# Performance work log

Measured on AMD Instinct MI355X. Metric: run time of the kernel, lower is better.

Reference implementation:

```python
import jax, jax.numpy as jnp
import numpy as np

N_NODES = 100000
N_TARGETS = 8192
HIDDEN = 128
HEADS = 4


def setup_inputs() -> dict:
    key = jax.random.key(0)
    ks = iter(jax.random.split(key, 40))
    d = {}
    d['feat0'] = jax.random.normal(next(ks), (50000, 512), jnp.float32)
    d['feat1'] = jax.random.normal(next(ks), (50000, 512), jnp.float32)
    d['node_idx0'] = jnp.arange(50000, dtype=jnp.int32)
    d['node_idx1'] = jnp.arange(50000, dtype=jnp.int32) + 50000
    for nt in ('m', 'd'):
        for p in ('0', '1'):
            d[f'eidx_{nt}{p}'] = jax.random.randint(next(ks), (100000, 3), 0, N_NODES, jnp.int32)
            d[f'etgt_{nt}{p}'] = jax.random.randint(next(ks), (100000,), 0, N_TARGETS, jnp.int32)
    s = lambda *sh: 0.05 * jax.random.normal(next(ks), sh, jnp.float32)
    d['W0'] = s(HIDDEN, 512); d['b0'] = jnp.zeros((HIDDEN,), jnp.float32)
    d['W1'] = s(HIDDEN, 512); d['b1'] = jnp.zeros((HIDDEN,), jnp.float32)
    for nt in ('m', 'd'):
        for p in ('0', '1'):
            d[f'Wr_{nt}{p}'] = s(HEADS * HIDDEN, HIDDEN)
            d[f'a_{nt}{p}'] = s(HEADS, HIDDEN)
        d[f'Ws_{nt}'] = s(128, HEADS * HIDDEN)
        d[f'bs_{nt}'] = jnp.zeros((128,), jnp.float32)
        d[f'vs_{nt}'] = s(128)
        d[f'Wo_{nt}'] = s(64, HEADS * HIDDEN)
        d[f'bo_{nt}'] = jnp.zeros((64,), jnp.float32)
    return d


def _metapath_agg(feats, eidx, etgt, Wr, attn):
    # feats: [N,H]; eidx: [E,L]; etgt: [E] in [0,T)
    E = eidx.shape[0]
    h = feats[eidx].mean(axis=1)                       # [E,H]  metapath-instance encoding ('linear' rnn_type)
    eft = (h @ Wr.T).reshape(E, HEADS, HIDDEN)         # [E,heads,H]
    e = jax.nn.leaky_relu(jnp.einsum('ehd,hd->eh', eft, attn), 0.2)
    m = jax.ops.segment_max(e, etgt, num_segments=N_TARGETS)
    ex = jnp.exp(e - m[etgt])
    den = jax.ops.segment_sum(ex, etgt, num_segments=N_TARGETS)
    alpha = ex / (den[etgt] + 1e-9)                    # segment softmax over instances per target
    out = jax.ops.segment_sum(eft * alpha[:, :, None], etgt, num_segments=N_TARGETS)
    return jax.nn.elu(out).reshape(N_TARGETS, HEADS * HIDDEN)


def _semantic(h_list, Ws, bs, vs):
    betas = jnp.stack([(jnp.tanh(h @ Ws.T + bs) @ vs).mean() for h in h_list])
    beta = jax.nn.softmax(betas)
    return jnp.einsum('p,pth->th', beta, jnp.stack(h_list))


def reference(feat0, feat1, node_idx0, node_idx1,
              eidx_m0, etgt_m0, eidx_m1, etgt_m1,
              eidx_d0, etgt_d0, eidx_d1, etgt_d1,
              W0, b0, W1, b1,
              Wr_m0, a_m0, Wr_m1, a_m1, Wr_d0, a_d0, Wr_d1, a_d1,
              Ws_m, bs_m, vs_m, Ws_d, bs_d, vs_d,
              Wo_m, bo_m, Wo_d, bo_d):
    # per-node-type linear transform scattered by type_mask
    tf = jnp.zeros((N_NODES, HIDDEN), feat0.dtype)
    tf = tf.at[node_idx0].set(feat0 @ W0.T + b0)
    tf = tf.at[node_idx1].set(feat1 @ W1.T + b1)
    # (feat_drop is identity in eval / dropout_rate handled deterministically)
    hm0 = _metapath_agg(tf, eidx_m0, etgt_m0, Wr_m0, a_m0)
    hm1 = _metapath_agg(tf, eidx_m1, etgt_m1, Wr_m1, a_m1)
    hd0 = _metapath_agg(tf, eidx_d0, etgt_d0, Wr_d0, a_d0)
    hd1 = _metapath_agg(tf, eidx_d1, etgt_d1, Wr_d1, a_d1)
    h_miRNA = _semantic([hm0, hm1], Ws_m, bs_m, vs_m)
    h_disease = _semantic([hd0, hd1], Ws_d, bs_d, vs_d)
    logits_miRNA = h_miRNA @ Wo_m.T + bo_m
    logits_disease = h_disease @ Wo_d.T + bo_d
    return (logits_miRNA, logits_disease, h_miRNA, h_disease)
```

## Files before the change

### kernel.cpp

```cpp
#include <hip/hip_runtime.h>
#include <hip/hip_bf16.h>
#include <math.h>


#define HIDDEN 128
#define HEADS 4
#define NTGT 8192
#define NEDGE 100000
#define NNODES 100000

typedef __attribute__((ext_vector_type(8))) short bf16x8;
typedef __attribute__((ext_vector_type(4))) float f32x4;

__device__ inline short b16(float f)
{
    union { __hip_bfloat16 h; short s; } u;
    u.h = __float2bfloat16(f);
    return u.s;
}

__device__ inline float bf2f(unsigned short u)
{
    union { unsigned int i; float f; } v;
    v.i = (unsigned int)u << 16;
    return v.f;
}

struct GArgs {
    const void* A[4];
    const unsigned short* B[4];
    const float* bias[4];
    void* C[4];
    const int* rowmap[4];
    const float* vs[4];
    float* sem[4];
};

__global__ __launch_bounds__(256, 4)
void tgemm(GArgs g, int M)
{
    __shared__ unsigned short lds[32 * 512];
    const int z = blockIdx.z;
    const float* Af = (const float*)g.A[z];
    const unsigned short* Bp = g.B[z];
    const float* bias = g.bias[z];
    const int* rowmap = g.rowmap[z];
    unsigned short* Ch = (unsigned short*)g.C[z];

    const int tid = threadIdx.x;
    const int w = tid >> 6, l = tid & 63;
    const int lr = l & 15, s4 = l >> 4;
    const int m0 = blockIdx.x * 32;

    auto stage4 = [&](int rbase) {
        float4 v[4][2];
        #pragma unroll
        for (int q = 0; q < 4; ++q) {
            int rg = min(m0 + rbase + q, M - 1);
            const float* rowp = Af + (size_t)rg * 512;
            v[q][0] = *(const float4*)(rowp + l * 4);
            v[q][1] = *(const float4*)(rowp + 256 + l * 4);
        }
        #pragma unroll
        for (int q = 0; q < 4; ++q) {
            int rl = rbase + q;
            int rx = rl & 7;
            #pragma unroll
            for (int hh = 0; hh < 2; ++hh) {
                uint2 pk;
                pk.x = (unsigned int)(unsigned short)b16(v[q][hh].x) |
                       ((unsigned int)(unsigned short)b16(v[q][hh].y) << 16);
                pk.y = (unsigned int)(unsigned short)b16(v[q][hh].z) |
                       ((unsigned int)(unsigned short)b16(v[q][hh].w) << 16);
                int G = hh * 32 + (l >> 1);
                int slot = (G & ~7) | ((G & 7) ^ rx);
                *(uint2*)((char*)lds + (size_t)rl * 1024 + slot * 16 + (l & 1) * 8) = pk;
            }
        }
    };
    stage4(w * 8);
    stage4(w * 8 + 4);

    const int i = w & 1;
    const int jb = (w >> 1) * 4;

    f32x4 acc[4];
    #pragma unroll
    for (int jj = 0; jj < 4; ++jj) acc[jj] = (f32x4){0.f, 0.f, 0.f, 0.f};

    bf16x8 bbA[4], bbB[4];
    auto LDB = [&](int c, bf16x8 (&bb)[4]) {
        #pragma unroll
        for (int jj = 0; jj < 4; ++jj)
            bb[jj] = *(const bf16x8*)(Bp + ((size_t)(c * 8 + jb + jj) * 64 + l) * 8);
    };

    LDB(0, bbA);
    __syncthreads();

    const int r = i * 16 + lr;
    const int rx = r & 7;

    #pragma unroll
    for (int c = 0; c < 16; ++c) {
        int G = 4 * c + s4;
        int slot = (G & ~7) | ((G & 7) ^ rx);
        bf16x8 a = *(const bf16x8*)((const char*)lds + (size_t)r * 1024 + slot * 16);
        if (c & 1) {
            if (c + 1 < 16) LDB(c + 1, bbA);
            #pragma unroll
            for (int jj = 0; jj < 4; ++jj)
                acc[jj] = __builtin_amdgcn_mfma_f32_16x16x32_bf16(a, bbB[jj], acc[jj], 0, 0, 0);
        } else {
            if (c + 1 < 16) LDB(c + 1, bbB);
            #pragma unroll
            for (int jj = 0; jj < 4; ++jj)
                acc[jj] = __builtin_amdgcn_mfma_f32_16x16x32_bf16(a, bbA[jj], acc[jj], 0, 0, 0);
        }
    }

    #pragma unroll
    for (int rr = 0; rr < 4; ++rr) {
        int gm = m0 + i * 16 + s4 * 4 + rr;
        if (gm >= M) continue;
        size_t crow = (size_t)rowmap[gm];
        #pragma unroll
        for (int jj = 0; jj < 4; ++jj) {
            int n = (jb + jj) * 16 + lr;
            Ch[crow * 128 + n] = (unsigned short)b16(acc[jj][rr] + bias[n]);
        }
    }
}

template<int EPI, int NF, int MI, bool AB16, bool C16, int NFS>
__global__ __launch_bounds__(256)
void mgemm(GArgs g, int lda, int ldc,
           int aOffY, int bOffY, int cOffY, int nOffY, int M, int K)
{
    __shared__ float red[4];
    const int z = blockIdx.z;
    const unsigned short* Bp = g.B[z] + (size_t)blockIdx.y * bOffY;
    const float* bias = g.bias[z];
    const int* rowmap = g.rowmap[z];
    const int nbase = blockIdx.y * nOffY;
    float* Cf = nullptr;
    unsigned short* Ch = nullptr;
    if (g.C[z]) {
        if (C16) Ch = (unsigned short*)g.C[z] + (size_t)blockIdx.y * cOffY;
        else     Cf = (float*)g.C[z] + (size_t)blockIdx.y * cOffY;
    }
    const float* Af = nullptr;
    const unsigned short* Ah = nullptr;
    if (AB16) Ah = (const unsigned short*)g.A[z] + (size_t)blockIdx.y * aOffY;
    else      Af = (const float*)g.A[z] + (size_t)blockIdx.y * aOffY;

    const int tid = threadIdx.x;
    const int w = tid >> 6, l = tid & 63;
    const int lr = l & 15, lk = (l >> 4) * 8;
    const int m0 = blockIdx.x * (MI * 64) + w * (MI * 16);

    f32x4 acc[MI][NF];
    #pragma unroll
    for (int i = 0; i < MI; ++i)
        #pragma unroll
        for (int j = 0; j < NF; ++j)
            acc[i][j] = (f32x4){0.f, 0.f, 0.f, 0.f};

    float4 af0[MI][2], af1[MI][2];
    bf16x8 ah0[MI], ah1[MI];
    bf16x8 bb0[NF], bb1[NF];

    auto LD = [&](int k0, float4 (&af)[MI][2], bf16x8 (&ah)[MI], bf16x8 (&bb)[NF]) {
        #pragma unroll
        for (int i = 0; i < MI; ++i) {
            int row = min(m0 + i * 16 + lr, M - 1);
            if (AB16) {
                ah[i] = *(const bf16x8*)(Ah + (size_t)row * lda + k0 + lk);
            } else {
                const float* p = Af + (size_t)row * lda + k0 + lk;
                af[i][0] = *(const float4*)p;
                af[i][1] = *(const float4*)(p + 4);
            }
        }
        #pragma unroll
        for (int j = 0; j < NF; ++j)
            bb[j] = *(const bf16x8*)(Bp + ((size_t)((k0 >> 5) * NFS + j) * 64 + l) * 8);
    };

    auto CMP = [&](float4 (&af)[MI][2], bf16x8 (&ah)[MI], bf16x8 (&bb)[NF]) {
        bf16x8 a[MI];
        #pragma unroll
        for (int i = 0; i < MI; ++i) {
            if (AB16) {
                a[i] = ah[i];
            } else {
                bf16x8 r;
                r[0] = b16(af[i][0].x); r[1] = b16(af[i][0].y);
                r[2] = b16(af[i][0].z); r[3] = b16(af[i][0].w);
                r[4] = b16(af[i][1].x); r[5] = b16(af[i][1].y);
                r[6] = b16(af[i][1].z); r[7] = b16(af[i][1].w);
                a[i] = r;
            }
        }
        #pragma unroll
        for (int j = 0; j < NF; ++j)
            #pragma unroll
            for (int i = 0; i < MI; ++i)
                acc[i][j] = __builtin_amdgcn_mfma_f32_16x16x32_bf16(a[i], bb[j], acc[i][j], 0, 0, 0);
    };

    LD(0, af0, ah0, bb0);
    for (int k0 = 0; k0 < K; k0 += 64) {
        LD(k0 + 32, af1, ah1, bb1);
        CMP(af0, ah0, bb0);
        if (k0 + 64 < K) LD(k0 + 64, af0, ah0, bb0);
        CMP(af1, ah1, bb1);
    }

    if (EPI == 2) {
        const float* vs = g.vs[z];
        float local = 0.f;
        #pragma unroll
        for (int i = 0; i < MI; ++i) {
            int rbase = m0 + i * 16 + (l >> 4) * 4;
            #pragma unroll
            for (int r = 0; r < 4; ++r) {
                if (rbase + r >= M) continue;
                #pragma unroll
                for (int j = 0; j < NF; ++j) {
                    int n = nbase + j * 16 + lr;
                    local += tanhf(acc[i][j][r] + bias[n]) * vs[n];
                }
            }
        }
        #pragma unroll
        for (int o = 32; o; o >>= 1) local += __shfl_xor(local, o, 64);
        if (l == 0) red[w] = local;
        __syncthreads();
        if (tid == 0) atomicAdd(g.sem[z], red[0] + red[1] + red[2] + red[3]);
        return;
    }

    #pragma unroll
    for (int i = 0; i < MI; ++i) {
        int rbase = m0 + i * 16 + (l >> 4) * 4;
        #pragma unroll
        for (int r = 0; r < 4; ++r) {
            int gm = rbase + r;
            if (gm >= M) continue;
            size_t crow = rowmap ? (size_t)rowmap[gm] : (size_t)gm;
            #pragma unroll
            for (int j = 0; j < NF; ++j) {
                int n = nbase + j * 16 + lr;
                float v = acc[i][j][r];
                if (EPI == 0 && bias) v += bias[n];
                if (EPI == 1) v = v > 0.f ? v : expm1f(v);
                if (C16) Ch[crow * (size_t)ldc + n] = (unsigned short)b16(v);
                else     Cf[crow * (size_t)ldc + n] = v;
            }
        }
    }
}

struct PackArgs {
    const float* src[22];
    unsigned short* dst[22];
    int n16[22], k32[22], ld[22];
};

__global__ __launch_bounds__(256)
void pack_kernel(PackArgs pa)
{
    int c = blockIdx.y;
    int idx = blockIdx.x * 256 + threadIdx.x;
    int tot = pa.n16[c] * pa.k32[c] * 64;
    if (idx >= tot) return;
    int l = idx & 63;
    int rest = idx >> 6;
    int j = rest % pa.n16[c];
    int k0 = rest / pa.n16[c];
    int row = j * 16 + (l & 15);
    int col = k0 * 32 + (l >> 4) * 8;
    const float* s = pa.src[c] + (size_t)row * pa.ld[c] + col;
    float4 u = *(const float4*)s;
    float4 v = *(const float4*)(s + 4);
    bf16x8 r;
    r[0] = b16(u.x); r[1] = b16(u.y); r[2] = b16(u.z); r[3] = b16(u.w);
    r[4] = b16(v.x); r[5] = b16(v.y); r[6] = b16(v.z); r[7] = b16(v.w);
    *(bf16x8*)(pa.dst[c] + (size_t)idx * 8) = r;
}

struct WattArgs { const float* Wr[4]; const float* a[4]; };

__global__ __launch_bounds__(256)
void watt_kernel(WattArgs wa, float* __restrict__ watt4)
{
    int idx = blockIdx.x * 256 + threadIdx.x;
    int mp = idx >> 9, rest = idx & 511, h = rest >> 7, k = rest & 127;
    const float* Wr = wa.Wr[mp];
    const float* a = wa.a[mp];
    float s = 0.f;
    #pragma unroll 4
    for (int d = 0; d < HIDDEN; ++d)
        s += a[h * HIDDEN + d] * Wr[(size_t)(h * HIDDEN + d) * HIDDEN + k];
    watt4[idx] = s;
}

__global__ __launch_bounds__(256)
void watt_pack(const float* __restrict__ watt4, unsigned short* __restrict__ dst)
{
    int idx = blockIdx.x * 256 + threadIdx.x;
    int f = idx >> 9;
    int r = idx & 511;
    int l = r >> 3;
    int c = r & 7;
    int row = l & 15;
    int col = f * 32 + ((l >> 4) << 3) + c;
    dst[idx] = (unsigned short)b16(watt4[row * 128 + col]);
}

struct EArgs { const int* eidx[4]; const int* etgt[4]; };

__global__ __launch_bounds__(256)
void hist_kernel(EArgs ea, int* __restrict__ cnt4, int E)
{
    int e = blockIdx.x * 256 + threadIdx.x;
    int mp = blockIdx.y;
    if (e < E) atomicAdd(&cnt4[mp * NTGT + ea.etgt[mp][e]], 1);
}

__global__ __launch_bounds__(256)
void scan_kernel(int* __restrict__ cnt4, int* __restrict__ rowptr4)
{
    int mp = blockIdx.x;
    int* cnt = cnt4 + mp * NTGT;
    int* rowptr = rowptr4 + mp * (NTGT + 1);
    __shared__ int part[256];
    int t = threadIdx.x;
    int vals[32];
    int s = 0;
    int base = t * 32;
    #pragma unroll
    for (int i = 0; i < 32; ++i) { vals[i] = cnt[base + i]; s += vals[i]; }
    part[t] = s;
    __syncthreads();
    for (int o = 1; o < 256; o <<= 1) {
        int v = (t >= o) ? part[t - o] : 0;
        __syncthreads();
        part[t] += v;
        __syncthreads();
    }
    int off = (t == 0) ? 0 : part[t - 1];
    #pragma unroll
    for (int i = 0; i < 32; ++i) { rowptr[base + i] = off; off += vals[i]; cnt[base + i] = 0; }
    if (t == 255) rowptr[NTGT] = off;
}

__global__ __launch_bounds__(256)
void scatter_esc(EArgs ea, const int* __restrict__ rowptr4,
                 int* __restrict__ cur4, uint4* __restrict__ rec4,
                 const float* __restrict__ snode, int E)
{
    int e = blockIdx.x * 256 + threadIdx.x;
    int mp = blockIdx.y;
    if (e >= E) return;
    int t = ea.etgt[mp][e];
    int pos = atomicAdd(&cur4[mp * NTGT + t], 1);
    int slot = rowptr4[mp * (NTGT + 1) + t] + pos;

    const int* eidx = ea.eidx[mp];
    int i0 = eidx[e * 3 + 0], i1 = eidx[e * 3 + 1], i2 = eidx[e * 3 + 2];
    float4 s0 = *(const float4*)(snode + (size_t)i0 * 16 + mp * 4);
    float4 s1 = *(const float4*)(snode + (size_t)i1 * 16 + mp * 4);
    float4 s2 = *(const float4*)(snode + (size_t)i2 * 16 + mp * 4);
    const float inv3 = 1.f / 3.f;
    float es[4];
    es[0] = (s0.x + s1.x + s2.x) * inv3;
    es[1] = (s0.y + s1.y + s2.y) * inv3;
    es[2] = (s0.z + s1.z + s2.z) * inv3;
    es[3] = (s0.w + s1.w + s2.w) * inv3;
    #pragma unroll
    for (int h = 0; h < 4; ++h) {
        float v = (es[h] >= 0.f) ? es[h] : 0.2f * es[h];
        es[h] = __expf(v);
    }
    uint4* rp = rec4 + ((size_t)mp * NEDGE + slot) * 2;
    rp[0] = make_uint4((unsigned)i0, (unsigned)i1, (unsigned)i2, 0u);
    *(float4*)&rp[1] = make_float4(es[0], es[1], es[2], es[3]);
}

__global__ __launch_bounds__(256)
void seg_kernel(const int* __restrict__ rowptr4, const uint4* __restrict__ rec4,
                const unsigned short* __restrict__ tfb,
                unsigned short* __restrict__ gnb)
{
    int mp = blockIdx.y;
    int w = threadIdx.x >> 6, l = threadIdx.x & 63;
    int t = blockIdx.x * 4 + w;
    const int* rp = rowptr4 + mp * (NTGT + 1);
    const uint4* rec = rec4 + (size_t)mp * NEDGE * 2;
    const unsigned short* tfl = tfb + 2 * l;

    int beg = rp[t], end = rp[t + 1];
    int n = end - beg;
    float den[4] = {0, 0, 0, 0}, aa[4] = {0, 0, 0, 0}, ab[4] = {0, 0, 0, 0};
    const float inv3 = 1.f / 3.f;

    if (n > 0) {
        int last = n - 1;
        auto LDI = [&](int j, uint4& ia, float4& wv) {
            int jj = min(j, last);
            ia = rec[(size_t)(beg + jj) * 2];
            wv = *(const float4*)&rec[(size_t)(beg + jj) * 2 + 1];
        };
        uint4 I0, I1, I2, I3, I4;
        float4 W0v, W1v, W2v, W3v, W4v;
        LDI(0, I0, W0v); LDI(1, I1, W1v); LDI(2, I2, W2v); LDI(3, I3, W3v);
        unsigned int x0 = *(const unsigned int*)(tfl + (size_t)I0.x * 128);
        unsigned int x1 = *(const unsigned int*)(tfl + (size_t)I0.y * 128);
        unsigned int x2 = *(const unsigned int*)(tfl + (size_t)I0.z * 128);
        unsigned int y0 = *(const unsigned int*)(tfl + (size_t)I1.x * 128);
        unsigned int y1 = *(const unsigned int*)(tfl + (size_t)I1.y * 128);
        unsigned int y2 = *(const unsigned int*)(tfl + (size_t)I1.z * 128);
        unsigned int z0 = *(const unsigned int*)(tfl + (size_t)I2.x * 128);
        unsigned int z1 = *(const unsigned int*)(tfl + (size_t)I2.y * 128);
        unsigned int z2 = *(const unsigned int*)(tfl + (size_t)I2.z * 128);
        for (int i = 0; i < n; ++i) {
            unsigned int w0 = *(const unsigned int*)(tfl + (size_t)I3.x * 128);
            unsigned int w1 = *(const unsigned int*)(tfl + (size_t)I3.y * 128);
            unsigned int w2 = *(const unsigned int*)(tfl + (size_t)I3.z * 128);
            LDI(i + 4, I4, W4v);
            float fa = (bf2f((unsigned short)x0) + bf2f((unsigned short)x1) +
                        bf2f((unsigned short)x2)) * inv3;
            float fb = (bf2f((unsigned short)(x0 >> 16)) + bf2f((unsigned short)(x1 >> 16)) +
                        bf2f((unsigned short)(x2 >> 16))) * inv3;
            float es[4] = {W0v.x, W0v.y, W0v.z, W0v.w};
            #pragma unroll
            for (int h = 0; h < 4; ++h) {
                den[h] += es[h]; aa[h] += es[h] * fa; ab[h] += es[h] * fb;
            }
            x0 = y0; x1 = y1; x2 = y2;
            y0 = z0; y1 = z1; y2 = z2;
            z0 = w0; z1 = w1; z2 = w2;
            I3 = I4;
            W0v = W1v; W1v = W2v; W2v = W3v; W3v = W4v;
        }
    }

    unsigned short* gr = gnb + ((size_t)mp * NTGT + t) * 512;
    #pragma unroll
    for (int h = 0; h < 4; ++h) {
        float d = 1.f / (den[h] + 1e-9f);
        unsigned int lo = (unsigned int)(unsigned short)b16(aa[h] * d);
        unsigned int hi = (unsigned int)(unsigned short)b16(ab[h] * d);
        *(unsigned int*)(gr + h * 128 + 2 * l) = lo | (hi << 16);
    }
}

__global__ void beta_kernel(const float* __restrict__ s, float* __restrict__ beta)
{
    int nt = threadIdx.x;
    if (nt < 2 && blockIdx.x == 0) {
        float b0 = s[nt * 2] * (1.f / 8192.f), b1 = s[nt * 2 + 1] * (1.f / 8192.f);
        float mm = fmaxf(b0, b1);
        float e0 = __expf(b0 - mm), e1 = __expf(b1 - mm);
        float d = e0 + e1;
        beta[nt * 2] = e0 / d;
        beta[nt * 2 + 1] = e1 / d;
    }
}

__global__ __launch_bounds__(256)
void combine_kernel(const unsigned short* __restrict__ obb,
                    const float* __restrict__ betab,
                    float* __restrict__ hout, unsigned short* __restrict__ hb)
{
    int nt = blockIdx.y;
    size_t i4 = ((size_t)blockIdx.x * 256 + threadIdx.x) * 4;
    const unsigned short* o0 = obb + (size_t)(2 * nt) * NTGT * 512 + i4;
    const unsigned short* o1 = obb + (size_t)(2 * nt + 1) * NTGT * 512 + i4;
    float b0 = betab[nt * 2], b1 = betab[nt * 2 + 1];
    uint2 xa = *(const uint2*)o0;
    uint2 xb = *(const uint2*)o1;
    float4 r;
    r.x = b0 * bf2f((unsigned short)xa.x)         + b1 * bf2f((unsigned short)xb.x);
    r.y = b0 * bf2f((unsigned short)(xa.x >> 16)) + b1 * bf2f((unsigned short)(xb.x >> 16));
    r.z = b0 * bf2f((unsigned short)xa.y)         + b1 * bf2f((unsigned short)xb.y);
    r.w = b0 * bf2f((unsigned short)(xa.y >> 16)) + b1 * bf2f((unsigned short)(xb.y >> 16));
    *(float4*)(hout + (size_t)nt * NTGT * 512 + i4) = r;
    unsigned int lo = (unsigned int)(unsigned short)b16(r.x) |
                      ((unsigned int)(unsigned short)b16(r.y) << 16);
    unsigned int hi = (unsigned int)(unsigned short)b16(r.z) |
                      ((unsigned int)(unsigned short)b16(r.w) << 16);
    *(uint2*)(hb + (size_t)nt * NTGT * 512 + i4) = make_uint2(lo, hi);
}

extern "C" void kernel_launch(void* const* d_in, const int* in_sizes, int n_in,
                              void* d_out, int out_size, void* d_ws, size_t ws_size,
                              hipStream_t stream)
{
    const float* feat0 = (const float*)d_in[0];
    const float* feat1 = (const float*)d_in[1];
    const int* nidx0 = (const int*)d_in[2];
    const int* nidx1 = (const int*)d_in[3];
    const int* eidx[4] = {(const int*)d_in[4], (const int*)d_in[6],
                          (const int*)d_in[8], (const int*)d_in[10]};
    const int* etgt[4] = {(const int*)d_in[5], (const int*)d_in[7],
                          (const int*)d_in[9], (const int*)d_in[11]};
    const float* W0 = (const float*)d_in[12]; const float* b0 = (const float*)d_in[13];
    const float* W1 = (const float*)d_in[14]; const float* b1 = (const float*)d_in[15];
    const float* Wr[4] = {(const float*)d_in[16], (const float*)d_in[18],
                          (const float*)d_in[25], (const float*)d_in[27]};
    const float* av[4] = {(const float*)d_in[17], (const float*)d_in[19],
                          (const float*)d_in[26], (const float*)d_in[28]};
    const float* Ws[2] = {(const float*)d_in[20], (const float*)d_in[29]};
    const float* bs[2] = {(const float*)d_in[21], (const float*)d_in[30]};
    const float* vsem[2] = {(const float*)d_in[22], (const float*)d_in[31]};
    const float* Wo[2] = {(const float*)d_in[23], (const float*)d_in[32]};
    const float* bo[2] = {(const float*)d_in[24], (const float*)d_in[33]};
    float* out = (float*)d_out;

    char* p = (char*)d_ws;
    auto carve = [&](size_t bytes) { char* r = p; p += (bytes + 255) & ~(size_t)255; return r; };
    unsigned short* tfb = (unsigned short*)carve((size_t)NNODES * 128 * 2);
    unsigned short* gnb = (unsigned short*)carve((size_t)4 * NTGT * 512 * 2);
    unsigned short* obb = (unsigned short*)carve((size_t)4 * NTGT * 512 * 2);
    unsigned short* hb  = (unsigned short*)carve((size_t)2 * NTGT * 512 * 2);
    float* snode        = (float*)carve((size_t)NNODES * 16 * 4);
    uint4* rec4         = (uint4*)carve((size_t)4 * NEDGE * 32);
    unsigned short* w0b = (unsigned short*)carve(65536 * 2);
    unsigned short* w1b = (unsigned short*)carve(65536 * 2);
    unsigned short* wrb = (unsigned short*)carve(4 * 65536 * 2);
    unsigned short* wsb = (unsigned short*)carve(2 * 65536 * 2);
    unsigned short* wob = (unsigned short*)carve(2 * 32768 * 2);
    unsigned short* wattp = (unsigned short*)carve(2048 * 2);
    float* watt4        = (float*)carve(4 * 512 * 4);
    float* ssem         = (float*)carve(4 * 4);
    float* betab        = (float*)carve(4 * 4);
    int* cnt4           = (int*)carve((size_t)4 * NTGT * 4);
    int* rowptr4        = (int*)carve((size_t)4 * (NTGT + 1) * 4);

    hipMemsetAsync(ssem, 0, 16, stream);
    hipMemsetAsync(cnt4, 0, (size_t)4 * NTGT * 4, stream);

    dim3 blk(256, 1, 1);

    PackArgs pa;
    pa.src[0] = W0; pa.dst[0] = w0b; pa.n16[0] = 8; pa.k32[0] = 16; pa.ld[0] = 512;
    pa.src[1] = W1; pa.dst[1] = w1b; pa.n16[1] = 8; pa.k32[1] = 16; pa.ld[1] = 512;
    for (int mp = 0; mp < 4; ++mp)
        for (int h = 0; h < 4; ++h) {
            int c = 2 + mp * 4 + h;
            pa.src[c] = Wr[mp] + (size_t)h * 128 * 128;
            pa.dst[c] = wrb + (size_t)(mp * 4 + h) * 16384;
            pa.n16[c] = 8; pa.k32[c] = 4; pa.ld[c] = 128;
        }
    pa.src[18] = Ws[0]; pa.dst[18] = wsb;         pa.n16[18] = 8; pa.k32[18] = 16; pa.ld[18] = 512;
    pa.src[19] = Ws[1]; pa.dst[19] = wsb + 65536; pa.n16[19] = 8; pa.k32[19] = 16; pa.ld[19] = 512;
    pa.src[20] = Wo[0]; pa.dst[20] = wob;         pa.n16[20] = 4; pa.k32[20] = 16; pa.ld[20] = 512;
    pa.src[21] = Wo[1]; pa.dst[21] = wob + 32768; pa.n16[21] = 4; pa.k32[21] = 16; pa.ld[21] = 512;
    pack_kernel<<<dim3(32, 22), blk, 0, stream>>>(pa);

    WattArgs wa;
    for (int mp = 0; mp < 4; ++mp) { wa.Wr[mp] = Wr[mp]; wa.a[mp] = av[mp]; }
    watt_kernel<<<dim3(8), blk, 0, stream>>>(wa, watt4);
    watt_pack<<<dim3(8), blk, 0, stream>>>(watt4, wattp);

    {
        GArgs g = {};
        g.A[0] = feat0; g.A[1] = feat1;
        g.B[0] = w0b;   g.B[1] = w1b;
        g.bias[0] = b0; g.bias[1] = b1;
        g.C[0] = tfb;   g.C[1] = tfb;
        g.rowmap[0] = nidx0; g.rowmap[1] = nidx1;
        tgemm<<<dim3(1563, 1, 2), blk, 0, stream>>>(g, 50000);
    }

    {
        GArgs g = {};
        g.A[0] = tfb;
        g.B[0] = wattp;
        g.C[0] = snode;
        mgemm<0, 1, 2, true, false, 1><<<dim3(782, 1, 1), blk, 0, stream>>>(
            g, 128, 16, 0, 0, 0, 0, NNODES, 128);
    }

    EArgs ea;
    for (int mp = 0; mp < 4; ++mp) { ea.eidx[mp] = eidx[mp]; ea.etgt[mp] = etgt[mp]; }

    hist_kernel<<<dim3(391, 4), blk, 0, stream>>>(ea, cnt4, NEDGE);
    scan_kernel<<<dim3(4), blk, 0, stream>>>(cnt4, rowptr4);
    scatter_esc<<<dim3(391, 4), blk, 0, stream>>>(ea, rowptr4, cnt4, rec4,
                                                  snode, NEDGE);
    seg_kernel<<<dim3(NTGT / 4, 4), blk, 0, stream>>>(rowptr4, rec4, tfb, gnb);

    const size_t LOG_OFF[2] = {0, (size_t)NTGT * 64};
    float* hout = out + (size_t)NTGT * 128;

    {
        GArgs g = {};
        for (int mp = 0; mp < 4; ++mp) {
            g.A[mp] = gnb + (size_t)mp * NTGT * 512;
            g.B[mp] = wrb + (size_t)mp * 65536;
            g.C[mp] = obb + (size_t)mp * NTGT * 512;
        }
        mgemm<1, 8, 2, true, true, 8><<<dim3(64, 4, 4), blk, 0, stream>>>(
            g, 512, 512, 128, 16384, 128, 0, NTGT, 128);
    }

    {
        GArgs g = {};
        for (int mp = 0; mp < 4; ++mp) {
            int nt = mp >> 1;
            g.A[mp] = obb + (size_t)mp * NTGT * 512;
            g.B[mp] = wsb + (size_t)nt * 65536;
            g.bias[mp] = bs[nt];
            g.vs[mp] = vsem[nt];
            g.sem[mp] = ssem + mp;
        }
        mgemm<2, 4, 1, true, false, 8><<<dim3(128, 2, 4), blk, 0, stream>>>(
            g, 512, 0, 0, 2048, 0, 64, NTGT, 512);
    }

    beta_kernel<<<dim3(1), dim3(64), 0, stream>>>(ssem, betab);
    combine_kernel<<<dim3(NTGT * 512 / 4 / 256, 2), blk, 0, stream>>>(obb, betab, hout, hb);

    {
        GArgs g = {};
        for (int nt = 0; nt < 2; ++nt) {
            g.A[nt] = hb + (size_t)nt * NTGT * 512;
            g.B[nt] = wob + (size_t)nt * 32768;
            g.bias[nt] = bo[nt];
            g.C[nt] = out + LOG_OFF[nt];
        }
        mgemm<0, 2, 1, true, false, 4><<<dim3(128, 2, 2), blk, 0, stream>>>(
            g, 512, 64, 0, 1024, 0, 32, NTGT, 512);
    }
}
```

Before: 292.7 us.

## Make feature-transform GEMM persistent with register-prefetched 16-row tiles

The tgemm kernel becomes a persistent grid of 1280 blocks that loop over 16-row tiles covering both feature matrices. Each block prefetches the next tile's fp32 rows into registers while running MFMA on the current tile in LDS, so global loads overlap with compute. Tiles shrink from 32 rows to 16, and each wave now computes two output column groups instead of four, with a higher occupancy hint. The trade-off is more B-matrix reloads per row and an extra barrier per tile. The bounds checks are dropped because the tile count divides the row count exactly.

```diff
diff --git a/kernel.cpp b/kernel.cpp
--- a/kernel.cpp
+++ b/kernel.cpp
@@ -8,6 +8,10 @@
 #define NTGT 8192
 #define NEDGE 100000
 #define NNODES 100000
+#define TROWS 16
+#define TPF 3125
+#define NTILES (2 * TPF)
+#define TGRID 1280
 
 typedef __attribute__((ext_vector_type(8))) short bf16x8;
 typedef __attribute__((ext_vector_type(4))) float f32x4;
@@ -36,99 +40,104 @@
     float* sem[4];
 };
 
-__global__ __launch_bounds__(256, 4)
-void tgemm(GArgs g, int M)
-{
-    __shared__ unsigned short lds[32 * 512];
-    const int z = blockIdx.z;
-    const float* Af = (const float*)g.A[z];
-    const unsigned short* Bp = g.B[z];
-    const float* bias = g.bias[z];
-    const int* rowmap = g.rowmap[z];
-    unsigned short* Ch = (unsigned short*)g.C[z];
-
+__global__ __launch_bounds__(256, 5)
+void tgemm(GArgs g)
+{
+    __shared__ unsigned short lds[TROWS * 512];
     const int tid = threadIdx.x;
     const int w = tid >> 6, l = tid & 63;
     const int lr = l & 15, s4 = l >> 4;
-    const int m0 = blockIdx.x * 32;
-
-    auto stage4 = [&](int rbase) {
-        float4 v[4][2];
-        #pragma unroll
-        for (int q = 0; q < 4; ++q) {
-            int rg = min(m0 + rbase + q, M - 1);
-            const float* rowp = Af + (size_t)rg * 512;
-            v[q][0] = *(const float4*)(rowp + l * 4);
-            v[q][1] = *(const float4*)(rowp + 256 + l * 4);
-        }
-        #pragma unroll
-        for (int q = 0; q < 4; ++q) {
-            int rl = rbase + q;
+    const int jb = w * 2;
+
+    float4 v[8];
+
+    auto LOADR = [&](int t) {
+        int z = (t >= TPF) ? 1 : 0;
+        const float* Af = (const float*)g.A[z];
+        int rowbase = (t - z * TPF) * TROWS;
+        #pragma unroll
+        for (int q = 0; q < 8; ++q) {
+            int rl = w * 4 + (q >> 1);
+            v[q] = *(const float4*)(Af + (size_t)(rowbase + rl) * 512 +
+                                    (q & 1) * 256 + l * 4);
+        }
+    };
+
+    auto WRLDS = [&]() {
+        #pragma unroll
+        for (int q = 0; q < 8; ++q) {
+            int rl = w * 4 + (q >> 1);
             int rx = rl & 7;
-            #pragma unroll
-            for (int hh = 0; hh < 2; ++hh) {
-                uint2 pk;
-                pk.x = (unsigned int)(unsigned short)b16(v[q][hh].x) |
-                       ((unsigned int)(unsigned short)b16(v[q][hh].y) << 16);
-                pk.y = (unsigned int)(unsigned short)b16(v[q][hh].z) |
-                       ((unsigned int)(unsigned short)b16(v[q][hh].w) << 16);
-                int G = hh * 32 + (l >> 1);
-                int slot = (G & ~7) | ((G & 7) ^ rx);
-                *(uint2*)((char*)lds + (size_t)rl * 1024 + slot * 16 + (l & 1) * 8) = pk;
+            uint2 pk;
+            pk.x = (unsigned)(unsigned short)b16(v[q].x) |
+                   ((unsigned)(unsigned short)b16(v[q].y) << 16);
+            pk.y = (unsigned)(unsigned short)b16(v[q].z) |
+                   ((unsigned)(unsigned short)b16(v[q].w) << 16);
+            int G = (q & 1) * 32 + (l >> 1);
+            int slot = (G & ~7) | ((G & 7) ^ rx);
+            *(uint2*)((char*)lds + (size_t)rl * 1024 + slot * 16 + (l & 1) * 8) = pk;
+        }
+    };
+
+    auto COMPUTE = [&](int t) {
+        int z = (t >= TPF) ? 1 : 0;
+        const unsigned short* Bp = g.B[z];
+        const float* bias = g.bias[z];
+        const int* rowmap = g.rowmap[z];
+        unsigned short* Ch = (unsigned short*)g.C[z];
+        int rowbase = (t - z * TPF) * TROWS;
+
+        f32x4 acc0 = (f32x4){0.f, 0.f, 0.f, 0.f};
+        f32x4 acc1 = (f32x4){0.f, 0.f, 0.f, 0.f};
+        bf16x8 bA0, bA1, bB0, bB1;
+        bA0 = *(const bf16x8*)(Bp + ((size_t)(jb + 0) * 64 + l) * 8);
+        bA1 = *(const bf16x8*)(Bp + ((size_t)(jb + 1) * 64 + l) * 8);
+        const int r = lr, rx = r & 7;
+        #pragma unroll
+        for (int c = 0; c < 16; ++c) {
+            int G = 4 * c + s4;
+            int slot = (G & ~7) | ((G & 7) ^ rx);
+            bf16x8 a = *(const bf16x8*)((const char*)lds + (size_t)r * 1024 + slot * 16);
+            if (c & 1) {
+                if (c < 15) {
+                    bA0 = *(const bf16x8*)(Bp + ((size_t)((c + 1) * 8 + jb + 0) * 64 + l) * 8);
+                    bA1 = *(const bf16x8*)(Bp + ((size_t)((c + 1) * 8 + jb + 1) * 64 + l) * 8);
+                }
+                acc0 = __builtin_amdgcn_mfma_f32_16x16x32_bf16(a, bB0, acc0, 0, 0, 0);
+                acc1 = __builtin_amdgcn_mfma_f32_16x16x32_bf16(a, bB1, acc1, 0, 0, 0);
+            } else {
+                if (c < 15) {
+                    bB0 = *(const bf16x8*)(Bp + ((size_t)((c + 1) * 8 + jb + 0) * 64 + l) * 8);
+                    bB1 = *(const bf16x8*)(Bp + ((size_t)((c + 1) * 8 + jb + 1) * 64 + l) * 8);
+                }
+                acc0 = __builtin_amdgcn_mfma_f32_16x16x32_bf16(a, bA0, acc0, 0, 0, 0);
+                acc1 = __builtin_amdgcn_mfma_f32_16x16x32_bf16(a, bA1, acc1, 0, 0, 0);
             }
         }
+        #pragma unroll
+        for (int rr = 0; rr < 4; ++rr) {
+            int gm = rowbase + s4 * 4 + rr;
+            size_t crow = (size_t)rowmap[gm];
+            Ch[crow * 128 + (jb + 0) * 16 + lr] =
+                (unsigned short)b16(acc0[rr] + bias[(jb + 0) * 16 + lr]);
+            Ch[crow * 128 + (jb + 1) * 16 + lr] =
+                (unsigned short)b16(acc1[rr] + bias[(jb + 1) * 16 + lr]);
+        }
     };
-    stage4(w * 8);
-    stage4(w * 8 + 4);
-
-    const int i = w & 1;
-    const int jb = (w >> 1) * 4;
-
-    f32x4 acc[4];
-    #pragma unroll
-    for (int jj = 0; jj < 4; ++jj) acc[jj] = (f32x4){0.f, 0.f, 0.f, 0.f};
-
-    bf16x8 bbA[4], bbB[4];
-    auto LDB = [&](int c, bf16x8 (&bb)[4]) {
-        #pragma unroll
-        for (int jj = 0; jj < 4; ++jj)
-            bb[jj] = *(const bf16x8*)(Bp + ((size_t)(c * 8 + jb + jj) * 64 + l) * 8);
-    };
-
-    LDB(0, bbA);
-    __syncthreads();
-
-    const int r = i * 16 + lr;
-    const int rx = r & 7;
-
-    #pragma unroll
-    for (int c = 0; c < 16; ++c) {
-        int G = 4 * c + s4;
-        int slot = (G & ~7) | ((G & 7) ^ rx);
-        bf16x8 a = *(const bf16x8*)((const char*)lds + (size_t)r * 1024 + slot * 16);
-        if (c & 1) {
-            if (c + 1 < 16) LDB(c + 1, bbA);
-            #pragma unroll
-            for (int jj = 0; jj < 4; ++jj)
-                acc[jj] = __builtin_amdgcn_mfma_f32_16x16x32_bf16(a, bbB[jj], acc[jj], 0, 0, 0);
-        } else {
-            if (c + 1 < 16) LDB(c + 1, bbB);
-            #pragma unroll
-            for (int jj = 0; jj < 4; ++jj)
-                acc[jj] = __builtin_amdgcn_mfma_f32_16x16x32_bf16(a, bbA[jj], acc[jj], 0, 0, 0);
-        }
-    }
-
-    #pragma unroll
-    for (int rr = 0; rr < 4; ++rr) {
-        int gm = m0 + i * 16 + s4 * 4 + rr;
-        if (gm >= M) continue;
-        size_t crow = (size_t)rowmap[gm];
-        #pragma unroll
-        for (int jj = 0; jj < 4; ++jj) {
-            int n = (jb + jj) * 16 + lr;
-            Ch[crow * 128 + n] = (unsigned short)b16(acc[jj][rr] + bias[n]);
-        }
+
+    int tile = blockIdx.x;
+    if (tile >= NTILES) return;
+    LOADR(tile);
+    while (true) {
+        WRLDS();
+        __syncthreads();
+        int next = tile + TGRID;
+        bool more = (next < NTILES);
+        if (more) LOADR(next);
+        COMPUTE(tile);
+        if (!more) break;
+        tile = next;
+        __syncthreads();
     }
 }
 
@@ -573,7 +582,7 @@
         g.bias[0] = b0; g.bias[1] = b1;
         g.C[0] = tfb;   g.C[1] = tfb;
         g.rowmap[0] = nidx0; g.rowmap[1] = nidx1;
-        tgemm<<<dim3(1563, 1, 2), blk, 0, stream>>>(g, 50000);
+        tgemm<<<dim3(TGRID), blk, 0, stream>>>(g);
     }
 
     {
```

After: 310.7 us. +6.1%, slower.
